# Kernel tuning notes

Measured on AMD Instinct MI355X. Metric: run time of the kernel, lower is better.

The kernel has to match this reference:

```python
import jax, jax.numpy as jnp
import numpy as np
import math

B, INST, C, HEADS, DH, CTX = 1, 4, 320, 8, 40, 768
FULL, HW = 512, 4096
SCALE = DH ** -0.5
EPS = 1e-5


def _ln(x, g, b):
    m = x.mean(-1, keepdims=True)
    v = ((x - m) ** 2).mean(-1, keepdims=True)
    return (x - m) / jnp.sqrt(v + EPS) * g + b


def _mha(x, ctx, Wq, Wk, Wv, Wo, bo, mask=None):
    # x: [b, n, C]; ctx: [b, m, ctx_dim]; mask: [b, n, m] bool (True = keep)
    b, n, _ = x.shape
    m = ctx.shape[1]
    q = (x @ Wq).reshape(b, n, HEADS, DH)
    k = (ctx @ Wk).reshape(b, m, HEADS, DH)
    v = (ctx @ Wv).reshape(b, m, HEADS, DH)
    sim = jnp.einsum('bihd,bjhd->bhij', q, k) * SCALE
    if mask is not None:
        sim = jnp.where(mask[:, None, :, :], sim, -jnp.finfo(sim.dtype).max)
    attn = jax.nn.softmax(sim, axis=-1)
    out = jnp.einsum('bhij,bjhd->bihd', attn, v).reshape(b, n, HEADS * DH)
    return out @ Wo + bo


def _fourier(x, num_freqs=8, temperature=100.0):
    freqs = temperature ** (jnp.arange(num_freqs, dtype=x.dtype) / num_freqs)
    parts = []
    for i in range(num_freqs):
        parts.append(jnp.sin(freqs[i] * x))
        parts.append(jnp.cos(freqs[i] * x))
    return jax.lax.stop_gradient(jnp.concatenate(parts, axis=-1))  # @torch.no_grad in source


def _resize(x, H, W):
    # torch F.interpolate bilinear, align_corners=False (half-pixel), no antialias
    return jax.image.resize(x, x.shape[:2] + (H, W), method='bilinear', antialias=False)


def setup_inputs() -> dict:
    key = jax.random.key(0)
    ks = jax.random.split(key, 32)
    s = 0.02
    inp = {
        'ca_x': jax.random.normal(ks[0], (B, INST + 1, HW, C), jnp.float32),
        'guidance_mask': jax.random.uniform(ks[1], (B, INST, FULL, FULL), jnp.float32),
        'supplement_mask': jax.random.uniform(ks[2], (B, 1, FULL, FULL), jnp.float32),
        'image_token': jax.random.normal(ks[3], (B, INST + 1, HW, C), jnp.float32),
        'context': jax.random.normal(ks[4], (INST + 1, 77, CTX), jnp.float32),
        'box': jax.random.uniform(ks[5], (B, INST, 8), jnp.float32),
        'img_features': jax.random.normal(ks[6], (B * INST, 257, CTX), jnp.float32),
        'bg_features': jax.random.normal(ks[7], (B, 257, CTX), jnp.float32),
        'sigmoid_values': jax.random.uniform(ks[8], (B, INST, FULL, FULL), jnp.float32),
        'Wq_obj': jax.random.normal(ks[9], (C, C), jnp.float32) * s,
        'Wk_obj': jax.random.normal(ks[10], (CTX, C), jnp.float32) * s,
        'Wv_obj': jax.random.normal(ks[11], (CTX, C), jnp.float32) * s,
        'Wo_obj': jax.random.normal(ks[12], (C, C), jnp.float32) * s,
        'bo_obj': jnp.zeros((C,), jnp.float32),
        'ln_g_obj': jnp.ones((C,), jnp.float32),
        'ln_b_obj': jnp.zeros((C,), jnp.float32),
        'Wq2': jax.random.normal(ks[13], (C, C), jnp.float32) * s,
        'Wk2': jax.random.normal(ks[14], (CTX, C), jnp.float32) * s,
        'Wv2': jax.random.normal(ks[15], (CTX, C), jnp.float32) * s,
        'Wo2': jax.random.normal(ks[16], (C, C), jnp.float32) * s,
        'bo2': jnp.zeros((C,), jnp.float32),
        'ln_g2': jnp.ones((C,), jnp.float32),
        'ln_b2': jnp.zeros((C,), jnp.float32),
        'pn_W1': jax.random.normal(ks[17], (128, 512), jnp.float32) * s,
        'pn_b1': jnp.zeros((512,), jnp.float32),
        'pn_W2': jax.random.normal(ks[18], (512, 512), jnp.float32) * s,
        'pn_b2': jnp.zeros((512,), jnp.float32),
        'pn_W3': jax.random.normal(ks[19], (512, CTX), jnp.float32) * s,
        'pn_b3': jnp.zeros((CTX,), jnp.float32),
        'la_Wq': jax.random.normal(ks[20], (C, C), jnp.float32) * s,
        'la_Wk': jax.random.normal(ks[21], (C, C), jnp.float32) * s,
        'la_Wv': jax.random.normal(ks[22], (C, C), jnp.float32) * s,
        'la_Wo': jax.random.normal(ks[23], (C, C), jnp.float32) * s,
        'la_bo': jnp.zeros((C,), jnp.float32),
        'height': FULL,
        'width': FULL,
    }
    return inp


def reference(ca_x, guidance_mask, supplement_mask, image_token, context, box,
              img_features, bg_features, sigmoid_values,
              Wq_obj, Wk_obj, Wv_obj, Wo_obj, bo_obj, ln_g_obj, ln_b_obj,
              Wq2, Wk2, Wv2, Wo2, bo2, ln_g2, ln_b2,
              pn_W1, pn_b1, pn_W2, pn_b2, pn_W3, pn_b3,
              la_Wq, la_Wk, la_Wv, la_Wo, la_bo,
              height, width):
    b, _, hw, c = ca_x.shape
    inst = guidance_mask.shape[1]
    down = int(math.sqrt(height * width // hw))
    H, W = height // down, width // down

    gm = _resize(guidance_mask, H, W)           # [B, inst, H, W]
    supp = _resize(supplement_mask, H, W)       # [B, 1, H, W]
    sig = _resize(sigmoid_values, H, W).reshape(b, inst, hw, 1)

    # PositionNet on boxes
    box_emb = _fourier(box.reshape(b * inst, 1, 8))          # [B*inst, 1, 128]
    h1 = jax.nn.silu(box_emb @ pn_W1 + pn_b1)
    h2 = jax.nn.silu(h1 @ pn_W2 + pn_b2)
    box_token = h2 @ pn_W3 + pn_b3                            # [B*inst, 1, 768]

    # foreground cross-attention (ea_obj)
    context_fg = jnp.concatenate([context[1:], img_features, box_token], axis=1)
    q_in = _ln(image_token[:, 1:].reshape(b * inst, hw, c), ln_g_obj, ln_b_obj)
    ea_x = _mha(q_in, context_fg, Wq_obj, Wk_obj, Wv_obj, Wo_obj, bo_obj)
    ea_x = ea_x.reshape(b, inst, hw, c) * sig

    ca_inst = ca_x[:, 1:] * sig + ea_x                        # [B, inst, HW, C]

    # background cross-attention (ea2)
    context_bg = jnp.concatenate([context[0:1], bg_features], axis=1)
    q2 = _ln(ca_inst.sum(axis=1).reshape(b, hw, c), ln_g2, ln_b2)
    ea_bg = _mha(q2, context_bg, Wq2, Wk2, Wv2, Wo2, bo2)     # [B, HW, C]
    ca0 = ca_x[:, 0] + ea_bg

    # layout self-attention with guidance-mask sparsity
    gm_all = jnp.concatenate([gm, supp], axis=1).reshape(b, inst + 1, hw)
    # sum over phases of outer products; clamp-to-1 in source only feeds the ==0 test
    sim_mask = jnp.einsum('bpi,bpj->bij', gm_all, gm_all) != 0  # [B, HW, HW] keep-mask
    fusion = _mha(image_token[:, 0], image_token[:, 0],
                  la_Wq, la_Wk, la_Wv, la_Wo, la_bo, mask=sim_mask)

    out = ca0 + ca_inst.sum(axis=1) + fusion                  # [B, HW, C]
    return out
```

## Files before the change

kernel.cpp:

```cpp
#include <hip/hip_runtime.h>
#include <hip/hip_bf16.h>
#include <math.h>

typedef unsigned short bhalf;
typedef unsigned int u32;
typedef unsigned long long u64;
typedef __attribute__((ext_vector_type(8))) short s16x8;
typedef __attribute__((ext_vector_type(4))) float f32x4;

#define SCALE_QK 0.15811388300841898f
#define K2E (SCALE_QK * 1.4426950408889634f)
#define NEG_INF (-3.402823466e38f)

__device__ __forceinline__ float bf2f(bhalf u){
    union { unsigned int i; float f; } v; v.i = ((unsigned int)u) << 16; return v.f;
}
__device__ __forceinline__ bhalf f2bf(float f){
    unsigned int x = __float_as_uint(f);
    unsigned int r = (x + 0x7fffu + ((x >> 16) & 1u)) >> 16;
    return (bhalf)r;
}
__device__ __forceinline__ float fexp2(float x){
    float r; asm("v_exp_f32 %0, %1" : "=v"(r) : "v"(x)); return r;
}
__device__ __forceinline__ u32 cvtpk(float lo, float hi){
    u32 r; asm("v_cvt_pk_bf16_f32 %0, %1, %2" : "=v"(r) : "v"(lo), "v"(hi)); return r;
}

struct WT12 { const float* in[12]; bhalf* out[12]; };

struct ProjArgs {
    const bhalf *q_in, *ctx_all, *x_la;
    const bhalf *wqobjT, *wkobjT, *wk2T, *lawqT, *wvobjT, *wv2T, *lawvT;
    bhalf *q_obj, *k_obj, *k_bg, *qkl, *vt_obj, *vt_bg, *vt_l;
};

template<int K>
__device__ __forceinline__ void gemm5x4_body(
    int bx, int by, const bhalf* __restrict__ A, const bhalf* __restrict__ Wt,
    bhalf* __restrict__ Cbf, int M, int kdm, float scale)
{
    const int wave = threadIdx.x >> 6, lane = threadIdx.x & 63;
    const int mb = bx * 256 + wave * 64;
    const int n0 = by * 64;
    const int klo = (lane >> 4) * 8;
    const bhalf* ap[4];
#pragma unroll
    for (int f = 0; f < 4; ++f){
        int mrow = mb + f * 16 + (lane & 15); if (mrow > M - 1) mrow = M - 1;
        ap[f] = A + (long)mrow * K + klo;
    }
    const bhalf* wp = Wt + (long)(n0 + (lane & 15)) * K + klo;
    const f32x4 fz = {0.f, 0.f, 0.f, 0.f};
    f32x4 acc[4][4];
#pragma unroll
    for (int f = 0; f < 4; ++f)
#pragma unroll
        for (int t = 0; t < 4; ++t) acc[f][t] = fz;
#pragma unroll
    for (int k0 = 0; k0 < K; k0 += 32){
        s16x8 av[4];
#pragma unroll
        for (int f = 0; f < 4; ++f) av[f] = *(const s16x8*)(ap[f] + k0);
        s16x8 bv[4];
#pragma unroll
        for (int t = 0; t < 4; ++t) bv[t] = *(const s16x8*)(wp + (long)t * 16 * K + k0);
#pragma unroll
        for (int f = 0; f < 4; ++f)
#pragma unroll
            for (int t = 0; t < 4; ++t)
                acc[f][t] = __builtin_amdgcn_mfma_f32_16x16x32_bf16(av[f], bv[t], acc[f][t], 0, 0, 0);
    }
#pragma unroll
    for (int f = 0; f < 4; ++f){
        const int rb = mb + f * 16 + ((threadIdx.x & 63) >> 4) * 4;
#pragma unroll
        for (int t = 0; t < 4; ++t){
            const int col = n0 + t * 16 + (threadIdx.x & 15);
            const int hh = col / 40, cc = col % 40;
#pragma unroll
            for (int r = 0; r < 4; ++r){
                const int row = rb + r;
                if (row >= M) continue;
                Cbf[(((long)(row / kdm) * 8 + hh) * kdm + (row % kdm)) * 40 + cc] = f2bf(acc[f][t][r] * scale);
            }
        }
    }
}

template<int K>
__device__ __forceinline__ void gemm_vt_body(
    int bx, int by, const bhalf* __restrict__ A, const bhalf* __restrict__ Wt,
    bhalf* __restrict__ Vt, int M, int vt_ns, int PAD, bhalf (*Tsh)[72])
{
    const int wave = threadIdx.x >> 6, lane = threadIdx.x & 63;
    const int m0 = bx * 64 + wave * 16;
    const int n0 = by * 64;
    int mrow = m0 + (lane & 15); if (mrow > M - 1) mrow = M - 1;
    const int klo = (lane >> 4) * 8;
    const bhalf* ap = A + (long)mrow * K + klo;
    const bhalf* wp = Wt + (long)(n0 + (lane & 15)) * K + klo;
    const f32x4 fz = {0.f, 0.f, 0.f, 0.f};
    f32x4 acc[4]; acc[0] = fz; acc[1] = fz; acc[2] = fz; acc[3] = fz;
#pragma unroll
    for (int k0 = 0; k0 < K; k0 += 32){
        s16x8 a = *(const s16x8*)(ap + k0);
#pragma unroll
        for (int t = 0; t < 4; ++t){
            s16x8 b = *(const s16x8*)(wp + (long)t * 16 * K + k0);
            acc[t] = __builtin_amdgcn_mfma_f32_16x16x32_bf16(a, b, acc[t], 0, 0, 0);
        }
    }
    const int hi = lane >> 4, l15 = lane & 15;
#pragma unroll
    for (int t = 0; t < 4; ++t)
#pragma unroll
        for (int r = 0; r < 4; ++r)
            Tsh[wave * 16 + hi * 4 + r][t * 16 + l15] = f2bf(acc[t][r]);
    __syncthreads();
    const int c = threadIdx.x & 63, jq = threadIdx.x >> 6;
    const int jbase = bx * 64 + jq * 16;
    if (jbase >= PAD) return;
    bhalf* vp = Vt + (long)(n0 + c) * vt_ns + jbase;
    if (jbase + 16 <= M){
        u32 wb[8];
#pragma unroll
        for (int p = 0; p < 8; ++p)
            wb[p] = (u32)Tsh[jq * 16 + 2 * p][c] | ((u32)Tsh[jq * 16 + 2 * p + 1][c] << 16);
        *(uint4*)vp       = make_uint4(wb[0], wb[1], wb[2], wb[3]);
        *(uint4*)(vp + 8) = make_uint4(wb[4], wb[5], wb[6], wb[7]);
    } else if (jbase >= M){
        *(uint4*)vp       = make_uint4(0, 0, 0, 0);
        *(uint4*)(vp + 8) = make_uint4(0, 0, 0, 0);
    } else {
        for (int jj = 0; jj < 16; ++jj)
            vp[jj] = (jbase + jj < M) ? Tsh[jq * 16 + jj][c] : (bhalf)0;
    }
}

struct PrepArgs {
    const float *itok, *g_obj, *b_obj; bhalf *q_in, *x_la;
    WT12 wt;
    const float *gmask, *smask, *sgv; float *gm_all, *sig;
    const float *box, *W1, *b1, *W2, *b2, *W3, *b3; float* tok;
};

__global__ __launch_bounds__(320) void mega_prep(PrepArgs a){
    __shared__ float smem[4160];
    const int bid = blockIdx.x, tid = threadIdx.x;
    if (bid < 16){
        float* emb = smem;
        float* h1  = smem + 128;
        float* h2  = smem + 640;
        float* red = smem + 1152;
        const int bb = bid >> 2, sl = bid & 3;
        const int lane = tid & 63, wv = tid >> 6;
        for (int t = tid; t < 128; t += 320){
            const int i = t >> 4, jj = t & 15, j = jj & 7;
            const float f = powf(100.f, (float)i * 0.125f);
            const float v = f * a.box[bb * 8 + j];
            emb[t] = (jj < 8) ? sinf(v) : cosf(v);
        }
        __syncthreads();
        {
            float acc[8] = {0, 0, 0, 0, 0, 0, 0, 0};
            for (int k = wv; k < 128; k += 5){
                const float e = emb[k];
                const float4 w0 = *(const float4*)(a.W1 + (long)k * 512 + lane * 8);
                const float4 w1 = *(const float4*)(a.W1 + (long)k * 512 + lane * 8 + 4);
                acc[0] += e * w0.x; acc[1] += e * w0.y; acc[2] += e * w0.z; acc[3] += e * w0.w;
                acc[4] += e * w1.x; acc[5] += e * w1.y; acc[6] += e * w1.z; acc[7] += e * w1.w;
            }
#pragma unroll
            for (int j = 0; j < 8; ++j) red[wv * 512 + lane * 8 + j] = acc[j];
            __syncthreads();
            for (int t = tid; t < 512; t += 320){
                const float s = a.b1[t] + red[t] + red[512 + t] + red[1024 + t] + red[1536 + t] + red[2048 + t];
                h1[t] = s / (1.f + __expf(-s));
            }
            __syncthreads();
        }
        {
            float acc[8] = {0, 0, 0, 0, 0, 0, 0, 0};
            for (int k = wv; k < 512; k += 5){
                const float e = h1[k];
                const float4 w0 = *(const float4*)(a.W2 + (long)k * 512 + lane * 8);
                const float4 w1 = *(const float4*)(a.W2 + (long)k * 512 + lane * 8 + 4);
                acc[0] += e * w0.x; acc[1] += e * w0.y; acc[2] += e * w0.z; acc[3] += e * w0.w;
                acc[4] += e * w1.x; acc[5] += e * w1.y; acc[6] += e * w1.z; acc[7] += e * w1.w;
            }
            __syncthreads();
#pragma unroll
            for (int j = 0; j < 8; ++j) red[wv * 512 + lane * 8 + j] = acc[j];
            __syncthreads();
            for (int t = tid; t < 512; t += 320){
                const float s = a.b2[t] + red[t] + red[512 + t] + red[1024 + t] + red[1536 + t] + red[2048 + t];
                h2[t] = s / (1.f + __expf(-s));
            }
            __syncthreads();
        }
        {
            float acc[3] = {0, 0, 0};
            const float* W3s = a.W3 + sl * 192;
            for (int k = wv; k < 512; k += 5){
                const float e = h2[k];
                const float* row = W3s + (long)k * 768 + lane * 3;
                acc[0] += e * row[0]; acc[1] += e * row[1]; acc[2] += e * row[2];
            }
            __syncthreads();
#pragma unroll
            for (int j = 0; j < 3; ++j) red[wv * 192 + lane * 3 + j] = acc[j];
            __syncthreads();
            for (int t = tid; t < 192; t += 320){
                const float s = a.b3[sl * 192 + t] + red[t] + red[192 + t] + red[384 + t] + red[576 + t] + red[768 + t];
                a.tok[bb * 768 + sl * 192 + t] = s;
            }
        }
    } else if (bid < 456){
        float (*T)[65] = (float(*)[65])smem;
        const int b = bid - 16;
        int w, t, K;
        if (b < 200){ w = b / 25; t = b % 25; K = 320; }
        else        { w = 8 + (b - 200) / 60; t = (b - 200) % 60; K = 768; }
        const int k0 = (t / 5) * 64, n0 = (t % 5) * 64;
        const float* in = a.wt.in[w];
        bhalf* out = a.wt.out[w];
        const int c = tid & 63, wv = tid >> 6;
        if (tid < 256){
#pragma unroll
            for (int r = 0; r < 16; ++r)
                T[wv + r * 4][c] = in[(long)(k0 + wv + r * 4) * 320 + n0 + c];
        }
        __syncthreads();
        if (tid < 256){
#pragma unroll
            for (int r = 0; r < 16; ++r)
                out[(long)(n0 + wv + r * 4) * K + k0 + c] = f2bf(T[c][wv + r * 4]);
        }
    } else if (bid < 600){
        if (tid < 256){
            const int b = bid - 456;
            const int p = b >> 4;
            const int i = (b & 15) * 256 + tid;
            const int y = i >> 6, x = i & 63;
            const int o = (8 * y + 3) * 512 + 8 * x + 3;
            const float* s; float* dst;
            if (p < 4){ s = a.gmask + (long)p * 262144; dst = a.gm_all + p * 4096; }
            else if (p == 4){ s = a.smask; dst = a.gm_all + 4 * 4096; }
            else { s = a.sgv + (long)(p - 5) * 262144; dst = a.sig + (p - 5) * 4096; }
            dst[i] = 0.25f * (s[o] + s[o + 1] + s[o + 512] + s[o + 513]);
        }
    } else {
        const int lane = tid & 63, wv = tid >> 6;
        const int wgid = (bid - 600) * 5 + wv;
        for (int row = wgid; row < 20480; row += 10240){
            if (row >= 16384){
                const int rr = row - 16384;
#pragma unroll
                for (int j = 0; j < 5; ++j){
                    const int c = lane + 64 * j;
                    a.x_la[(long)rr * 320 + c] = f2bf(a.itok[(long)rr * 320 + c]);
                }
                continue;
            }
            float v[5];
            float s = 0.f, sq = 0.f;
#pragma unroll
            for (int j = 0; j < 5; ++j){
                v[j] = a.itok[(long)(4096 + row) * 320 + lane + 64 * j];
                s += v[j]; sq += v[j] * v[j];
            }
#pragma unroll
            for (int o = 1; o < 64; o <<= 1){ s += __shfl_xor(s, o); sq += __shfl_xor(sq, o); }
            const float mean = s * (1.f / 320.f);
            const float var  = sq * (1.f / 320.f) - mean * mean;
            const float inv  = rsqrtf(var + 1e-5f);
#pragma unroll
            for (int j = 0; j < 5; ++j){
                const int c = lane + 64 * j;
                a.q_in[(long)row * 320 + c] = f2bf((v[j] - mean) * inv * a.g_obj[c] + a.b_obj[c]);
            }
        }
    }
}

__global__ __launch_bounds__(256) void mega_mask(
    const float* __restrict__ gm_all, u64* __restrict__ mb,
    const float* __restrict__ context, const float* __restrict__ imgf,
    const float* __restrict__ bgf, const float* __restrict__ boxtok, bhalf* __restrict__ out,
    ProjArgs a)
{
    __shared__ float smem[5440];
    const int tid = threadIdx.x;
    const int r = blockIdx.x;
    if (r < 256){
        const int i0 = (r & 63) << 6, j0 = (r >> 6) << 10;
        float* gi = smem;
        float* gj = smem + 320;
        for (int idx = tid; idx < 5 * 64; idx += 256)
            gi[idx] = gm_all[(idx >> 6) * 4096 + i0 + (idx & 63)];
        for (int idx = tid; idx < 5 * 1024; idx += 256)
            gj[idx] = gm_all[(idx >> 10) * 4096 + j0 + (idx & 1023)];
        __syncthreads();
        const int lane = tid & 63, wave = tid >> 6;
        const float a0 = gi[lane], a1 = gi[64 + lane], a2 = gi[128 + lane],
                    a3 = gi[192 + lane], a4 = gi[256 + lane];
        for (int ww = wave; ww < 16; ww += 4){
            u64 m = 0;
            for (int j = 0; j < 64; ++j){
                const int jj = (ww << 6) + j;
                const float dot = a0 * gj[jj] + a1 * gj[1024 + jj] + a2 * gj[2048 + jj]
                                + a3 * gj[3072 + jj] + a4 * gj[4096 + jj];
                m |= (u64)(dot != 0.f) << j;
            }
            mb[(long)((j0 >> 6) + ww) * 4096 + (i0 + lane)] = m;
        }
    } else if (r < 5296){
        const int idx = (r - 256) * 256 + tid;
        const int i = idx / (336 * 768);
        const int rr = (idx / 768) % 336;
        const int c = idx % 768;
        float v;
        if (i < 4){
            if (rr < 77)       v = context[((long)(1 + i) * 77 + rr) * 768 + c];
            else if (rr < 334) v = imgf[((long)i * 257 + (rr - 77)) * 768 + c];
            else if (rr == 334) v = boxtok[i * 768 + c];
            else v = 0.f;
        } else {
            if (rr < 77)       v = context[(long)rr * 768 + c];
            else if (rr < 334) v = bgf[(long)(rr - 77) * 768 + c];
            else v = 0.f;
        }
        out[idx] = f2bf(v);
    } else if (r < 5616){
        const int s = r - 5296;
        gemm5x4_body<320>(s % 64, s / 64, a.q_in, a.wqobjT, a.q_obj, 16384, 4096, K2E);
    } else if (r < 5776){
        const int s = r - 5616; const int by = s / 16, bx = s % 16;
        gemm5x4_body<320>(bx, by, a.x_la, a.lawqT, a.qkl, 4096, 4096, by < 5 ? K2E : 1.f);
    } else {
        const int s = r - 5776;
        bhalf (*Tsh)[72] = (bhalf(*)[72])smem;
        gemm_vt_body<320>(s % 64, s / 64, a.x_la, a.lawvT, a.vt_l, 4096, 4096, 4096, Tsh);
    }
}

__global__ __launch_bounds__(256) void proj_ctx(ProjArgs a){
    __shared__ bhalf Tsh[64][72];
    const int r = blockIdx.x;
    if (r < 30)       gemm5x4_body<768>(r % 6, r / 6, a.ctx_all, a.wkobjT, a.k_obj, 1344, 336, 1.f);
    else if (r < 40){ const int s = r - 30; gemm5x4_body<768>(s % 2, s / 2, a.ctx_all + (size_t)4 * 336 * 768, a.wk2T, a.k_bg, 336, 336, 1.f); }
    else { const int s = r - 40; const int bz = s / 30, rem = s % 30;
        if (bz == 4) gemm_vt_body<768>(rem % 6, rem / 6, a.ctx_all + (size_t)4 * 336 * 768, a.wv2T, a.vt_bg, 336, 384, 384, Tsh);
        else gemm_vt_body<768>(rem % 6, rem / 6, a.ctx_all + (size_t)bz * 336 * 768, a.wvobjT, a.vt_obj + (size_t)bz * 320 * 384, 336, 384, 384, Tsh);
    }
}

__global__ __launch_bounds__(256) void ln_rows_kernel(
    const float* __restrict__ in, const float* __restrict__ g, const float* __restrict__ b,
    bhalf* __restrict__ out)
{
    const int lane = threadIdx.x & 63;
    const int wgid = blockIdx.x * 4 + (threadIdx.x >> 6);
    for (int row = wgid; row < 4096; row += 4096){
        float v[5];
        float s = 0.f, sq = 0.f;
#pragma unroll
        for (int j = 0; j < 5; ++j){
            v[j] = in[(long)row * 320 + lane + 64 * j];
            s += v[j]; sq += v[j] * v[j];
        }
#pragma unroll
        for (int o = 1; o < 64; o <<= 1){ s += __shfl_xor(s, o); sq += __shfl_xor(sq, o); }
        const float mean = s * (1.f / 320.f);
        const float var  = sq * (1.f / 320.f) - mean * mean;
        const float inv  = rsqrtf(var + 1e-5f);
#pragma unroll
        for (int j = 0; j < 5; ++j){
            const int c = lane + 64 * j;
            out[(long)row * 320 + c] = f2bf((v[j] - mean) * inv * g[c] + b[c]);
        }
    }
}

template<int MODE>
__global__ __launch_bounds__(256) void gemm320(
    const bhalf* __restrict__ A, const bhalf* __restrict__ Wt,
    const float* __restrict__ bias, bhalf* __restrict__ Cbf,
    float* __restrict__ Cf, const float* __restrict__ add1, const float* __restrict__ add2,
    int M, int kdm, float ascale,
    const bhalf* __restrict__ A2, const bhalf* __restrict__ Wt2, const float* __restrict__ bias2)
{
    constexpr int K = 320;
    const int wave = threadIdx.x >> 6, lane = threadIdx.x & 63;
    const int m0 = blockIdx.x * 64 + wave * 16;
    const int n0 = blockIdx.y * 64;
    int mrow = m0 + (lane & 15); if (mrow > M - 1) mrow = M - 1;
    const int klo = (lane >> 4) * 8;
    const bhalf* ap = A + (long)mrow * K + klo;
    const bhalf* wp = Wt + (long)(n0 + (lane & 15)) * K + klo;
    const f32x4 fz = {0.f, 0.f, 0.f, 0.f};
    f32x4 acc[4]; acc[0] = fz; acc[1] = fz; acc[2] = fz; acc[3] = fz;
#pragma unroll
    for (int k0 = 0; k0 < K; k0 += 32){
        s16x8 a = *(const s16x8*)(ap + k0);
#pragma unroll
        for (int t = 0; t < 4; ++t){
            s16x8 b = *(const s16x8*)(wp + (long)t * 16 * K + k0);
            acc[t] = __builtin_amdgcn_mfma_f32_16x16x32_bf16(a, b, acc[t], 0, 0, 0);
        }
    }
    if (MODE == 6){
        const bhalf* ap2 = A2 + (long)mrow * K + klo;
        const bhalf* wp2 = Wt2 + (long)(n0 + (lane & 15)) * K + klo;
#pragma unroll
        for (int k0 = 0; k0 < K; k0 += 32){
            s16x8 a = *(const s16x8*)(ap2 + k0);
#pragma unroll
            for (int t = 0; t < 4; ++t){
                s16x8 b = *(const s16x8*)(wp2 + (long)t * 16 * K + k0);
                acc[t] = __builtin_amdgcn_mfma_f32_16x16x32_bf16(a, b, acc[t], 0, 0, 0);
            }
        }
    }
    if (MODE == 8){
#pragma unroll
        for (int i = 1; i < 4; ++i){
            const bhalf* api = A + (long)i * kdm + (long)mrow * K + klo;
#pragma unroll
            for (int k0 = 0; k0 < K; k0 += 32){
                s16x8 a = *(const s16x8*)(api + k0);
#pragma unroll
                for (int t = 0; t < 4; ++t){
                    s16x8 b = *(const s16x8*)(wp + (long)t * 16 * K + k0);
                    acc[t] = __builtin_amdgcn_mfma_f32_16x16x32_bf16(a, b, acc[t], 0, 0, 0);
                }
            }
        }
    }
    const int rb = m0 + (lane >> 4) * 4;
    int rin[4], rn[4];
    if (MODE == 5){
#pragma unroll
        for (int r = 0; r < 4; ++r){ const int row = rb + r; rin[r] = row / kdm; rn[r] = row % kdm; }
    }
#pragma unroll
    for (int t = 0; t < 4; ++t){
        const int col = n0 + t * 16 + (lane & 15);
        const int hh = col / 40, cc = col % 40;
#pragma unroll
        for (int r = 0; r < 4; ++r){
            const int row = rb + r;
            if (row >= M) continue;
            const float v = acc[t][r];
            if (MODE == 5)
                Cbf[(((long)rin[r] * 8 + hh) * kdm + rn[r]) * 40 + cc] = f2bf(v * ascale);
            else if (MODE == 6){
                const long o = (long)row * 320 + col;
                Cf[o] = v + bias[col] + bias2[col] + add1[o] + add2[o];
            }
            else if (MODE == 8){
                const long o = (long)row * 320 + col;
                float ssum = 0.f, cax = 0.f;
#pragma unroll
                for (int i = 0; i < 4; ++i){
                    const float sg = add2[i * 4096 + row];
                    ssum += sg;
                    cax += sg * add1[(long)i * 4096 * 320 + o];
                }
                Cf[o] = v + ssum * bias[col] + cax;
            }
        }
    }
}

template<bool GMM, bool PARTIAL, bool SIG>
__global__ __launch_bounds__(256) void flash4(
    const bhalf* __restrict__ Qh, const bhalf* __restrict__ Kh, const bhalf* __restrict__ Vt,
    bhalf* __restrict__ O, const u64* __restrict__ maskb,
    int NKV, long qh_is, long qh_hs, long kh_is, long kh_hs, long vt_is, int vt_ns, long o_is,
    const float* __restrict__ sigp, bhalf* __restrict__ pacc, float* __restrict__ pl)
{
    const int lane = threadIdx.x & 63, wave = threadIdx.x >> 6;
    const int l15 = lane & 15, hi = lane >> 4, klo = hi * 8;
    const int h = blockIdx.y;
    const int inst = PARTIAL ? 0 : blockIdx.z;
    const int g = PARTIAL ? blockIdx.z : 0;
    const int qbase = blockIdx.x * 256 + wave * 64;
    const s16x8 z8 = {0, 0, 0, 0, 0, 0, 0, 0};
    const f32x4 fz = {0.f, 0.f, 0.f, 0.f};

    s16x8 qa0[4], qa1[4];
#pragma unroll
    for (int qg = 0; qg < 4; ++qg){
        const bhalf* qp = Qh + inst * qh_is + h * qh_hs + (long)(qbase + qg * 16 + l15) * 40;
        qa0[qg] = *(const s16x8*)(qp + klo);
        qa1[qg] = (hi == 0) ? *(const s16x8*)(qp + 32) : z8;
    }
    const int krbase = 8 * (l15 >> 2) + (l15 & 3);
    const bhalf* khead = Kh + inst * kh_is + h * kh_hs;
    const bhalf* kbase = khead + (long)krbase * 40;

    const bhalf* vbase[3];
#pragma unroll
    for (int ct = 0; ct < 3; ++ct){
        int dr = h * 40 + ct * 16 + l15; if (dr > 319) dr = 319;
        vbase[ct] = Vt + inst * vt_is + (long)dr * vt_ns + hi * 8;
    }

    f32x4 acc[4][3];
    float l_run[4];
#pragma unroll
    for (int qg = 0; qg < 4; ++qg){
        acc[qg][0] = fz; acc[qg][1] = fz; acc[qg][2] = fz;
        l_run[qg] = 0.f;
    }

    auto soft_pv = [&](f32x4 (&d)[4], s16x8 (&vb)[3][2], float& lr, f32x4 (&ac)[3]){
        float csum = 0.f;
#pragma unroll
        for (int t = 0; t < 4; ++t)
#pragma unroll
            for (int r = 0; r < 4; ++r){
                const float p = fexp2(d[t][r]);
                d[t][r] = p; csum += p;
            }
        csum += __shfl_xor(csum, 16);
        csum += __shfl_xor(csum, 32);
        lr += csum;
#pragma unroll
        for (int s = 0; s < 2; ++s){
            union { u32 w[4]; s16x8 v; } pb;
            pb.w[0] = cvtpk(d[2 * s][0], d[2 * s][1]);
            pb.w[1] = cvtpk(d[2 * s][2], d[2 * s][3]);
            pb.w[2] = cvtpk(d[2 * s + 1][0], d[2 * s + 1][1]);
            pb.w[3] = cvtpk(d[2 * s + 1][2], d[2 * s + 1][3]);
#pragma unroll
            for (int ct = 0; ct < 3; ++ct)
                ac[ct] = __builtin_amdgcn_mfma_f32_16x16x32_bf16(vb[ct][s], pb.v, ac[ct], 0, 0, 0);
        }
    };

    const int ch0 = PARTIAL ? g * 8 : 0;
    const int chN = PARTIAL ? ch0 + 8 : (NKV >> 6);
    for (int ch = ch0; ch < chN; ++ch){
        const int c0 = ch << 6;
        s16x8 k0[4], k1[4];
#pragma unroll
        for (int t = 0; t < 4; ++t){
            const int toff = ((t >> 1) << 5) + ((t & 1) << 2);
            const bhalf* kp = kbase + (long)(c0 + toff) * 40;
            k0[t] = *(const s16x8*)(kp + klo);
            k1[t] = (hi == 0) ? *(const s16x8*)(kp + 32) : z8;
        }
        s16x8 vb[3][2];
#pragma unroll
        for (int ct = 0; ct < 3; ++ct)
#pragma unroll
            for (int s = 0; s < 2; ++s)
                vb[ct][s] = *(const s16x8*)(vbase[ct] + c0 + 32 * s);
        u64 M[4];
        if (GMM){
#pragma unroll
            for (int qg = 0; qg < 4; ++qg)
                M[qg] = maskb[(long)ch * 4096 + qbase + qg * 16 + l15];
        }
#pragma unroll
        for (int qg = 0; qg < 4; ++qg){
            f32x4 d[4];
#pragma unroll
            for (int t = 0; t < 4; ++t){
                d[t] = __builtin_amdgcn_mfma_f32_16x16x32_bf16(k0[t], qa0[qg], fz, 0, 0, 0);
                d[t] = __builtin_amdgcn_mfma_f32_16x16x32_bf16(k1[t], qa1[qg], d[t], 0, 0, 0);
            }
            if (GMM && !__all(M[qg] == ~0ull)){
                const u64 Mh = M[qg] >> (hi * 8);
#pragma unroll
                for (int t = 0; t < 4; ++t){
                    const int tb = ((t >> 1) << 5) + ((t & 1) << 2);
#pragma unroll
                    for (int r = 0; r < 4; ++r)
                        if (!((Mh >> (tb + r)) & 1)) d[t][r] = NEG_INF;
                }
            }
            soft_pv(d, vb, l_run[qg], acc[qg]);
        }
    }
    if (!PARTIAL && (NKV & 63)){
        const int c0 = (NKV >> 6) << 6;
        s16x8 k0[4], k1[4];
#pragma unroll
        for (int t = 0; t < 4; ++t){
            const int toff = ((t >> 1) << 5) + ((t & 1) << 2);
            int kr = c0 + toff + krbase; if (kr > NKV - 1) kr = NKV - 1;
            const bhalf* kp = khead + (long)kr * 40;
            k0[t] = *(const s16x8*)(kp + klo);
            k1[t] = (hi == 0) ? *(const s16x8*)(kp + 32) : z8;
        }
        s16x8 vb[3][2];
#pragma unroll
        for (int ct = 0; ct < 3; ++ct)
#pragma unroll
            for (int s = 0; s < 2; ++s)
                vb[ct][s] = *(const s16x8*)(vbase[ct] + c0 + 32 * s);
#pragma unroll
        for (int qg = 0; qg < 4; ++qg){
            f32x4 d[4];
#pragma unroll
            for (int t = 0; t < 4; ++t){
                d[t] = __builtin_amdgcn_mfma_f32_16x16x32_bf16(k0[t], qa0[qg], fz, 0, 0, 0);
                d[t] = __builtin_amdgcn_mfma_f32_16x16x32_bf16(k1[t], qa1[qg], d[t], 0, 0, 0);
            }
#pragma unroll
            for (int t = 0; t < 4; ++t){
                const int tb = ((t >> 1) << 5) + ((t & 1) << 2);
#pragma unroll
                for (int r = 0; r < 4; ++r)
                    if (c0 + tb + hi * 8 + r >= NKV) d[t][r] = NEG_INF;
            }
            soft_pv(d, vb, l_run[qg], acc[qg]);
        }
    }

    if (PARTIAL){
#pragma unroll
        for (int qg = 0; qg < 4; ++qg){
            const int q = qbase + qg * 16 + l15;
#pragma unroll
            for (int ct = 0; ct < 3; ++ct){
                bhalf* pb = pacc + ((((size_t)(g * 8 + h) * 3 + ct) * 4 + hi) * 4096 + q) * 4;
                uint2 w;
                w.x = cvtpk(acc[qg][ct][0], acc[qg][ct][1]);
                w.y = cvtpk(acc[qg][ct][2], acc[qg][ct][3]);
                *(uint2*)pb = w;
            }
            if (hi == 0)
                pl[(size_t)(g * 8 + h) * 4096 + q] = l_run[qg];
        }
    } else {
#pragma unroll
        for (int qg = 0; qg < 4; ++qg){
            const int q = qbase + qg * 16 + l15;
            float sc = 1.f / l_run[qg];
            if (SIG) sc *= sigp[(long)inst * 4096 + q];
            bhalf* op = O + inst * o_is + (long)q * 320 + h * 40;
#pragma unroll
            for (int ct = 0; ct < 3; ++ct){
                const int d0 = ct * 16 + hi * 4;
                if (d0 < 40){
                    uint2 w;
                    w.x = cvtpk(acc[qg][ct][0] * sc, acc[qg][ct][1] * sc);
                    w.y = cvtpk(acc[qg][ct][2] * sc, acc[qg][ct][3] * sc);
                    *(uint2*)(op + d0) = w;
                }
            }
        }
    }
}

__global__ __launch_bounds__(256) void combine_kernel(
    const bhalf* __restrict__ pacc, const float* __restrict__ pl, bhalf* __restrict__ O)
{
    const int idx = blockIdx.x * 256 + threadIdx.x;
    const int h = idx / (3 * 4096);
    const int r2 = idx % (3 * 4096);
    const int ct = r2 >> 12, q = r2 & 4095;
    float ls = 0.f;
#pragma unroll
    for (int g = 0; g < 8; ++g) ls += pl[(size_t)(g * 8 + h) * 4096 + q];
    float acc[16];
#pragma unroll
    for (int d = 0; d < 16; ++d) acc[d] = 0.f;
#pragma unroll
    for (int g = 0; g < 8; ++g){
#pragma unroll
        for (int hi = 0; hi < 4; ++hi){
            const ushort4 v = *(const ushort4*)(pacc + ((((size_t)(g * 8 + h) * 3 + ct) * 4 + hi) * 4096 + q) * 4);
            acc[hi * 4 + 0] += bf2f(v.x);
            acc[hi * 4 + 1] += bf2f(v.y);
            acc[hi * 4 + 2] += bf2f(v.z);
            acc[hi * 4 + 3] += bf2f(v.w);
        }
    }
    const float inv = 1.f / ls;
    bhalf* op = O + (size_t)q * 320 + h * 40 + ct * 16;
    if (ct < 2){
        u32 wb[8];
#pragma unroll
        for (int d = 0; d < 8; ++d) wb[d] = cvtpk(acc[2 * d] * inv, acc[2 * d + 1] * inv);
        *(uint4*)op       = make_uint4(wb[0], wb[1], wb[2], wb[3]);
        *(uint4*)(op + 8) = make_uint4(wb[4], wb[5], wb[6], wb[7]);
    } else {
        u32 wb[4];
#pragma unroll
        for (int d = 0; d < 4; ++d) wb[d] = cvtpk(acc[2 * d] * inv, acc[2 * d + 1] * inv);
        *(uint4*)op = make_uint4(wb[0], wb[1], wb[2], wb[3]);
    }
}

extern "C" void kernel_launch(void* const* d_in, const int* in_sizes, int n_in,
                              void* d_out, int out_size, void* d_ws, size_t ws_size,
                              hipStream_t stream)
{
    (void)in_sizes; (void)n_in; (void)out_size; (void)ws_size;
    const float* ca_x   = (const float*)d_in[0];
    const float* gmask  = (const float*)d_in[1];
    const float* smask  = (const float*)d_in[2];
    const float* itok   = (const float*)d_in[3];
    const float* ctx    = (const float*)d_in[4];
    const float* box    = (const float*)d_in[5];
    const float* imgf   = (const float*)d_in[6];
    const float* bgf    = (const float*)d_in[7];
    const float* sgv    = (const float*)d_in[8];
    const float* Wq_obj = (const float*)d_in[9];
    const float* Wk_obj = (const float*)d_in[10];
    const float* Wv_obj = (const float*)d_in[11];
    const float* Wo_obj = (const float*)d_in[12];
    const float* bo_obj = (const float*)d_in[13];
    const float* g_obj  = (const float*)d_in[14];
    const float* b_obj  = (const float*)d_in[15];
    const float* Wq2    = (const float*)d_in[16];
    const float* Wk2    = (const float*)d_in[17];
    const float* Wv2    = (const float*)d_in[18];
    const float* Wo2    = (const float*)d_in[19];
    const float* bo2    = (const float*)d_in[20];
    const float* g2     = (const float*)d_in[21];
    const float* b2     = (const float*)d_in[22];
    const float* pnW1   = (const float*)d_in[23];
    const float* pnb1   = (const float*)d_in[24];
    const float* pnW2   = (const float*)d_in[25];
    const float* pnb2   = (const float*)d_in[26];
    const float* pnW3   = (const float*)d_in[27];
    const float* pnb3   = (const float*)d_in[28];
    const float* laWq   = (const float*)d_in[29];
    const float* laWk   = (const float*)d_in[30];
    const float* laWv   = (const float*)d_in[31];
    const float* laWo   = (const float*)d_in[32];
    const float* labo   = (const float*)d_in[33];

    char* wsp = (char*)d_ws; size_t off = 0;
    auto alloc = [&](size_t bytes) -> void* {
        void* p = wsp + off; off += (bytes + 255) & ~(size_t)255; return p;
    };
    bhalf* wqobjT = (bhalf*)alloc(320 * 320 * 2);
    bhalf* woobjT = (bhalf*)alloc(320 * 320 * 2);
    bhalf* wq2T   = (bhalf*)alloc(320 * 320 * 2);
    bhalf* wo2T   = (bhalf*)alloc(320 * 320 * 2);
    bhalf* lawqT  = (bhalf*)alloc(320 * 320 * 2);
    bhalf* lawkT  = (bhalf*)alloc(320 * 320 * 2);
    bhalf* lawvT  = (bhalf*)alloc(320 * 320 * 2);
    bhalf* lawoT  = (bhalf*)alloc(320 * 320 * 2);
    bhalf* wkobjT = (bhalf*)alloc(768 * 320 * 2);
    bhalf* wvobjT = (bhalf*)alloc(768 * 320 * 2);
    bhalf* wk2T   = (bhalf*)alloc(768 * 320 * 2);
    bhalf* wv2T   = (bhalf*)alloc(768 * 320 * 2);
    float* gm_all = (float*)alloc(5 * 4096 * 4);
    float* sig    = (float*)alloc(4 * 4096 * 4);
    float* boxtok = (float*)alloc(4 * 768 * 4);
    u64*   maskb  = (u64*)alloc((size_t)64 * 4096 * 8);
    bhalf* ctx_all= (bhalf*)alloc((size_t)5 * 336 * 768 * 2);
    bhalf* q_in   = (bhalf*)alloc((size_t)16384 * 320 * 2);
    bhalf* x_la   = (bhalf*)alloc((size_t)4096 * 320 * 2);
    bhalf* k_obj  = (bhalf*)alloc((size_t)4 * 336 * 320 * 2);
    bhalf* vt_obj = (bhalf*)alloc((size_t)4 * 320 * 384 * 2);
    bhalf* k_bg   = (bhalf*)alloc((size_t)336 * 320 * 2);
    bhalf* vt_bg  = (bhalf*)alloc((size_t)320 * 384 * 2);
    bhalf* q_obj  = (bhalf*)alloc((size_t)16384 * 320 * 2);
    bhalf* o_obj  = (bhalf*)alloc((size_t)16384 * 320 * 2);
    float* Sbuf   = (float*)alloc((size_t)4096 * 320 * 4);
    bhalf* q2v    = (bhalf*)alloc((size_t)4096 * 320 * 2);
    bhalf* q2p    = (bhalf*)alloc((size_t)4096 * 320 * 2);
    bhalf* o2     = (bhalf*)alloc((size_t)4096 * 320 * 2);
    bhalf* qkl    = (bhalf*)alloc((size_t)2 * 4096 * 320 * 2);
    bhalf* vt_l   = (bhalf*)alloc((size_t)320 * 4096 * 2);
    bhalf* ol     = (bhalf*)alloc((size_t)4096 * 320 * 2);

    bhalf* pacc = (bhalf*)q_in;
    float* pl   = (float*)(pacc + (size_t)8 * 8 * 3 * 4 * 4096 * 4);

    PrepArgs pa{};
    pa.itok = itok; pa.g_obj = g_obj; pa.b_obj = b_obj; pa.q_in = q_in; pa.x_la = x_la;
    pa.wt.in[0] = Wq_obj; pa.wt.out[0] = wqobjT;
    pa.wt.in[1] = Wo_obj; pa.wt.out[1] = woobjT;
    pa.wt.in[2] = Wq2;    pa.wt.out[2] = wq2T;
    pa.wt.in[3] = Wo2;    pa.wt.out[3] = wo2T;
    pa.wt.in[4] = laWq;   pa.wt.out[4] = lawqT;
    pa.wt.in[5] = laWk;   pa.wt.out[5] = lawkT;
    pa.wt.in[6] = laWv;   pa.wt.out[6] = lawvT;
    pa.wt.in[7] = laWo;   pa.wt.out[7] = lawoT;
    pa.wt.in[8] = Wk_obj; pa.wt.out[8] = wkobjT;
    pa.wt.in[9] = Wv_obj; pa.wt.out[9] = wvobjT;
    pa.wt.in[10] = Wk2;   pa.wt.out[10] = wk2T;
    pa.wt.in[11] = Wv2;   pa.wt.out[11] = wv2T;
    pa.gmask = gmask; pa.smask = smask; pa.sgv = sgv; pa.gm_all = gm_all; pa.sig = sig;
    pa.box = box; pa.W1 = pnW1; pa.b1 = pnb1; pa.W2 = pnW2; pa.b2 = pnb2; pa.W3 = pnW3; pa.b3 = pnb3;
    pa.tok = boxtok;
    mega_prep<<<dim3(2648), 320, 0, stream>>>(pa);

    ProjArgs pj{};
    pj.q_in = q_in; pj.ctx_all = ctx_all; pj.x_la = x_la;
    pj.wqobjT = wqobjT; pj.wkobjT = wkobjT; pj.wk2T = wk2T; pj.lawqT = lawqT;
    pj.wvobjT = wvobjT; pj.wv2T = wv2T; pj.lawvT = lawvT;
    pj.q_obj = q_obj; pj.k_obj = k_obj; pj.k_bg = k_bg; pj.qkl = qkl;
    pj.vt_obj = vt_obj; pj.vt_bg = vt_bg; pj.vt_l = vt_l;

    mega_mask<<<dim3(6096), 256, 0, stream>>>(gm_all, maskb, ctx, imgf, bgf, boxtok, ctx_all, pj);

    proj_ctx<<<dim3(190), 256, 0, stream>>>(pj);

    flash4<false, false, true><<<dim3(16, 8, 4), 256, 0, stream>>>(q_obj, k_obj, vt_obj, o_obj, nullptr,
        335, (long)8 * 4096 * 40, (long)4096 * 40, (long)8 * 336 * 40, (long)336 * 40,
        (long)320 * 384, 384, (long)4096 * 320, sig, nullptr, nullptr);

    gemm320<8><<<dim3(64, 5), 256, 0, stream>>>(o_obj, woobjT, bo_obj, nullptr, Sbuf,
        ca_x + (size_t)4096 * 320, sig, 4096, 4096 * 320, 1.f, nullptr, nullptr, nullptr);

    ln_rows_kernel<<<dim3(1024), 256, 0, stream>>>(Sbuf, g2, b2, q2v);

    gemm320<5><<<dim3(64, 5), 256, 0, stream>>>(q2v, wq2T, nullptr, q2p, nullptr, nullptr, nullptr,
        4096, 4096, K2E, nullptr, nullptr, nullptr);

    flash4<false, false, false><<<dim3(16, 8, 1), 256, 0, stream>>>(q2p, k_bg, vt_bg, o2, nullptr,
        334, 0, (long)4096 * 40, 0, (long)336 * 40, 0, 384, 0, nullptr, nullptr, nullptr);

    flash4<true, true, false><<<dim3(16, 8, 8), 256, 0, stream>>>(qkl, qkl + (size_t)8 * 4096 * 40, vt_l, nullptr, maskb,
        4096, 0, (long)4096 * 40, 0, (long)4096 * 40, 0, 4096, 0, nullptr, pacc, pl);

    combine_kernel<<<dim3(384), 256, 0, stream>>>(pacc, pl, ol);

    gemm320<6><<<dim3(64, 5), 256, 0, stream>>>(o2, wo2T, bo2, nullptr, (float*)d_out, ca_x, Sbuf,
        4096, 1, 1.f, ol, lawoT, labo);
}
```

Before: 323.8 us.

## Split box position-net MLP across more blocks and kernels to shorten critical path

The three-layer box MLP previously ran serially inside 16 blocks of the prep kernel and was likely a long-tail straggler. Layer 1 now runs on 32 blocks in mega_prep, layer 2 on 32 extra blocks in mega_mask, and layer 3 in a new small kernel that writes the box token straight into ctx_all as bf16. This spreads the weight reads over more CUs. In exchange it adds a kernel launch and round-trips the intermediates through global memory.

```diff
diff --git a/kernel.cpp b/kernel.cpp
--- a/kernel.cpp
+++ b/kernel.cpp
@@ -142,19 +142,16 @@
     const float *itok, *g_obj, *b_obj; bhalf *q_in, *x_la;
     WT12 wt;
     const float *gmask, *smask, *sgv; float *gm_all, *sig;
-    const float *box, *W1, *b1, *W2, *b2, *W3, *b3; float* tok;
+    const float *box, *W1, *b1; float* h1g;
 };
 
 __global__ __launch_bounds__(320) void mega_prep(PrepArgs a){
     __shared__ float smem[4160];
     const int bid = blockIdx.x, tid = threadIdx.x;
-    if (bid < 16){
+    if (bid < 32){
         float* emb = smem;
-        float* h1  = smem + 128;
-        float* h2  = smem + 640;
-        float* red = smem + 1152;
-        const int bb = bid >> 2, sl = bid & 3;
-        const int lane = tid & 63, wv = tid >> 6;
+        float* red = smem + 128;
+        const int bb = bid >> 3, c0 = (bid & 7) * 64;
         for (int t = tid; t < 128; t += 320){
             const int i = t >> 4, jj = t & 15, j = jj & 7;
             const float f = powf(100.f, (float)i * 0.125f);
@@ -162,63 +159,21 @@
             emb[t] = (jj < 8) ? sinf(v) : cosf(v);
         }
         __syncthreads();
-        {
-            float acc[8] = {0, 0, 0, 0, 0, 0, 0, 0};
-            for (int k = wv; k < 128; k += 5){
-                const float e = emb[k];
-                const float4 w0 = *(const float4*)(a.W1 + (long)k * 512 + lane * 8);
-                const float4 w1 = *(const float4*)(a.W1 + (long)k * 512 + lane * 8 + 4);
-                acc[0] += e * w0.x; acc[1] += e * w0.y; acc[2] += e * w0.z; acc[3] += e * w0.w;
-                acc[4] += e * w1.x; acc[5] += e * w1.y; acc[6] += e * w1.z; acc[7] += e * w1.w;
-            }
-#pragma unroll
-            for (int j = 0; j < 8; ++j) red[wv * 512 + lane * 8 + j] = acc[j];
-            __syncthreads();
-            for (int t = tid; t < 512; t += 320){
-                const float s = a.b1[t] + red[t] + red[512 + t] + red[1024 + t] + red[1536 + t] + red[2048 + t];
-                h1[t] = s / (1.f + __expf(-s));
-            }
-            __syncthreads();
-        }
-        {
-            float acc[8] = {0, 0, 0, 0, 0, 0, 0, 0};
-            for (int k = wv; k < 512; k += 5){
-                const float e = h1[k];
-                const float4 w0 = *(const float4*)(a.W2 + (long)k * 512 + lane * 8);
-                const float4 w1 = *(const float4*)(a.W2 + (long)k * 512 + lane * 8 + 4);
-                acc[0] += e * w0.x; acc[1] += e * w0.y; acc[2] += e * w0.z; acc[3] += e * w0.w;
-                acc[4] += e * w1.x; acc[5] += e * w1.y; acc[6] += e * w1.z; acc[7] += e * w1.w;
-            }
-            __syncthreads();
-#pragma unroll
-            for (int j = 0; j < 8; ++j) red[wv * 512 + lane * 8 + j] = acc[j];
-            __syncthreads();
-            for (int t = tid; t < 512; t += 320){
-                const float s = a.b2[t] + red[t] + red[512 + t] + red[1024 + t] + red[1536 + t] + red[2048 + t];
-                h2[t] = s / (1.f + __expf(-s));
-            }
-            __syncthreads();
-        }
-        {
-            float acc[3] = {0, 0, 0};
-            const float* W3s = a.W3 + sl * 192;
-            for (int k = wv; k < 512; k += 5){
-                const float e = h2[k];
-                const float* row = W3s + (long)k * 768 + lane * 3;
-                acc[0] += e * row[0]; acc[1] += e * row[1]; acc[2] += e * row[2];
-            }
-            __syncthreads();
-#pragma unroll
-            for (int j = 0; j < 3; ++j) red[wv * 192 + lane * 3 + j] = acc[j];
-            __syncthreads();
-            for (int t = tid; t < 192; t += 320){
-                const float s = a.b3[sl * 192 + t] + red[t] + red[192 + t] + red[384 + t] + red[576 + t] + red[768 + t];
-                a.tok[bb * 768 + sl * 192 + t] = s;
-            }
-        }
-    } else if (bid < 456){
+        if (tid < 256){
+            const int kg = tid >> 6, c = tid & 63;
+            float acc = 0.f;
+            for (int k = kg; k < 128; k += 4)
+                acc += emb[k] * a.W1[(long)k * 512 + c0 + c];
+            red[kg * 64 + c] = acc;
+        }
+        __syncthreads();
+        if (tid < 64){
+            const float s = a.b1[c0 + tid] + red[tid] + red[64 + tid] + red[128 + tid] + red[192 + tid];
+            a.h1g[bb * 512 + c0 + tid] = s / (1.f + __expf(-s));
+        }
+    } else if (bid < 472){
         float (*T)[65] = (float(*)[65])smem;
-        const int b = bid - 16;
+        const int b = bid - 32;
         int w, t, K;
         if (b < 200){ w = b / 25; t = b % 25; K = 320; }
         else        { w = 8 + (b - 200) / 60; t = (b - 200) % 60; K = 768; }
@@ -237,9 +192,9 @@
             for (int r = 0; r < 16; ++r)
                 out[(long)(n0 + wv + r * 4) * K + k0 + c] = f2bf(T[c][wv + r * 4]);
         }
-    } else if (bid < 600){
+    } else if (bid < 616){
         if (tid < 256){
-            const int b = bid - 456;
+            const int b = bid - 472;
             const int p = b >> 4;
             const int i = (b & 15) * 256 + tid;
             const int y = i >> 6, x = i & 63;
@@ -252,7 +207,7 @@
         }
     } else {
         const int lane = tid & 63, wv = tid >> 6;
-        const int wgid = (bid - 600) * 5 + wv;
+        const int wgid = (bid - 616) * 5 + wv;
         for (int row = wgid; row < 20480; row += 10240){
             if (row >= 16384){
                 const int rr = row - 16384;
@@ -287,8 +242,9 @@
 __global__ __launch_bounds__(256) void mega_mask(
     const float* __restrict__ gm_all, u64* __restrict__ mb,
     const float* __restrict__ context, const float* __restrict__ imgf,
-    const float* __restrict__ bgf, const float* __restrict__ boxtok, bhalf* __restrict__ out,
-    ProjArgs a)
+    const float* __restrict__ bgf, bhalf* __restrict__ out, ProjArgs a,
+    const float* __restrict__ W2, const float* __restrict__ b2,
+    const float* __restrict__ h1g, float* __restrict__ h2g)
 {
     __shared__ float smem[5440];
     const int tid = threadIdx.x;
@@ -324,7 +280,6 @@
         if (i < 4){
             if (rr < 77)       v = context[((long)(1 + i) * 77 + rr) * 768 + c];
             else if (rr < 334) v = imgf[((long)i * 257 + (rr - 77)) * 768 + c];
-            else if (rr == 334) v = boxtok[i * 768 + c];
             else v = 0.f;
         } else {
             if (rr < 77)       v = context[(long)rr * 768 + c];
@@ -338,10 +293,50 @@
     } else if (r < 5776){
         const int s = r - 5616; const int by = s / 16, bx = s % 16;
         gemm5x4_body<320>(bx, by, a.x_la, a.lawqT, a.qkl, 4096, 4096, by < 5 ? K2E : 1.f);
-    } else {
+    } else if (r < 6096){
         const int s = r - 5776;
         bhalf (*Tsh)[72] = (bhalf(*)[72])smem;
         gemm_vt_body<320>(s % 64, s / 64, a.x_la, a.lawvT, a.vt_l, 4096, 4096, 4096, Tsh);
+    } else {
+        const int s = r - 6096;
+        const int bb = s >> 3, c0 = (s & 7) * 64;
+        float* h1s = smem;
+        float* red = smem + 512;
+        for (int t = tid; t < 512; t += 256) h1s[t] = h1g[bb * 512 + t];
+        __syncthreads();
+        const int kg = tid >> 6, c = tid & 63;
+        float acc = 0.f;
+        for (int k = kg; k < 512; k += 4)
+            acc += h1s[k] * W2[(long)k * 512 + c0 + c];
+        red[kg * 64 + c] = acc;
+        __syncthreads();
+        if (tid < 64){
+            const float sv = b2[c0 + tid] + red[tid] + red[64 + tid] + red[128 + tid] + red[192 + tid];
+            h2g[bb * 512 + c0 + tid] = sv / (1.f + __expf(-sv));
+        }
+    }
+}
+
+__global__ __launch_bounds__(256) void posnet_l3(
+    const float* __restrict__ h2g, const float* __restrict__ W3, const float* __restrict__ b3,
+    bhalf* __restrict__ ctx_all)
+{
+    __shared__ float smem[768];
+    const int bb = blockIdx.x / 12, c0 = (blockIdx.x % 12) * 64;
+    float* h2s = smem;
+    float* red = smem + 512;
+    const int tid = threadIdx.x;
+    for (int t = tid; t < 512; t += 256) h2s[t] = h2g[bb * 512 + t];
+    __syncthreads();
+    const int kg = tid >> 6, c = tid & 63;
+    float acc = 0.f;
+    for (int k = kg; k < 512; k += 4)
+        acc += h2s[k] * W3[(long)k * 768 + c0 + c];
+    red[kg * 64 + c] = acc;
+    __syncthreads();
+    if (tid < 64){
+        const float s = b3[c0 + tid] + red[tid] + red[64 + tid] + red[128 + tid] + red[192 + tid];
+        ctx_all[(size_t)bb * 336 * 768 + (size_t)334 * 768 + c0 + tid] = f2bf(s);
     }
 }
 
@@ -756,7 +751,8 @@
     bhalf* wv2T   = (bhalf*)alloc(768 * 320 * 2);
     float* gm_all = (float*)alloc(5 * 4096 * 4);
     float* sig    = (float*)alloc(4 * 4096 * 4);
-    float* boxtok = (float*)alloc(4 * 768 * 4);
+    float* h1g    = (float*)alloc(4 * 512 * 4);
+    float* h2g    = (float*)alloc(4 * 512 * 4);
     u64*   maskb  = (u64*)alloc((size_t)64 * 4096 * 8);
     bhalf* ctx_all= (bhalf*)alloc((size_t)5 * 336 * 768 * 2);
     bhalf* q_in   = (bhalf*)alloc((size_t)16384 * 320 * 2);
@@ -793,9 +789,8 @@
     pa.wt.in[10] = Wk2;   pa.wt.out[10] = wk2T;
     pa.wt.in[11] = Wv2;   pa.wt.out[11] = wv2T;
     pa.gmask = gmask; pa.smask = smask; pa.sgv = sgv; pa.gm_all = gm_all; pa.sig = sig;
-    pa.box = box; pa.W1 = pnW1; pa.b1 = pnb1; pa.W2 = pnW2; pa.b2 = pnb2; pa.W3 = pnW3; pa.b3 = pnb3;
-    pa.tok = boxtok;
-    mega_prep<<<dim3(2648), 320, 0, stream>>>(pa);
+    pa.box = box; pa.W1 = pnW1; pa.b1 = pnb1; pa.h1g = h1g;
+    mega_prep<<<dim3(2664), 320, 0, stream>>>(pa);
 
     ProjArgs pj{};
     pj.q_in = q_in; pj.ctx_all = ctx_all; pj.x_la = x_la;
@@ -804,7 +799,10 @@
     pj.q_obj = q_obj; pj.k_obj = k_obj; pj.k_bg = k_bg; pj.qkl = qkl;
     pj.vt_obj = vt_obj; pj.vt_bg = vt_bg; pj.vt_l = vt_l;
 
-    mega_mask<<<dim3(6096), 256, 0, stream>>>(gm_all, maskb, ctx, imgf, bgf, boxtok, ctx_all, pj);
+    mega_mask<<<dim3(6128), 256, 0, stream>>>(gm_all, maskb, ctx, imgf, bgf, ctx_all, pj,
+                                              pnW2, pnb2, h1g, h2g);
+
+    posnet_l3<<<dim3(48), 256, 0, stream>>>(h2g, pnW3, pnb3, ctx_all);
 
     proj_ctx<<<dim3(190), 256, 0, stream>>>(pj);
 
```

New measurement: 326.7 us. No clear change (+0.9%).
